# Performance work log

Hardware: AMD Instinct MI355X
Metric: run time of the kernel (lower is better)

## Reference

```python
import jax, jax.numpy as jnp
import numpy as np

B, S, H = 2, 256, 512
EPS = 1e-12  # TPLinker conditional LayerNorm default epsilon
NEG = -1e30  # finite stand-in for -inf in running max


def _cond_layer_norm(x, cond, Wg, Wb, gamma, beta):
    # TPLinker conditional LayerNorm: gamma/beta are modulated by a linear map of cond.
    g = gamma + cond @ Wg          # (..., H)
    b = beta + cond @ Wb           # (..., H)
    xc = x - jnp.mean(x, axis=-1, keepdims=True)
    inv = jax.lax.rsqrt(jnp.mean(xc * xc, axis=-1, keepdims=True) + EPS)
    return xc * inv * g + b


def setup_inputs() -> dict:
    key = jax.random.key(0)
    ks = jax.random.split(key, 6)
    return {
        "seq_hiddens": jax.random.normal(ks[0], (B, S, H), jnp.float32),
        "mask": jnp.ones((B, S), jnp.float32),
        "lamtha": jax.random.uniform(ks[1], (H,), jnp.float32),
        "Wg1": jax.random.normal(ks[2], (H, H), jnp.float32) * 0.02,
        "Wb1": jax.random.normal(ks[3], (H, H), jnp.float32) * 0.02,
        "g1": jnp.ones((H,), jnp.float32),
        "b1": jnp.zeros((H,), jnp.float32),
        "Wg2": jax.random.normal(ks[4], (H, H), jnp.float32) * 0.02,
        "Wb2": jax.random.normal(ks[5], (H, H), jnp.float32) * 0.02,
        "g2": jnp.ones((H,), jnp.float32),
        "b2": jnp.zeros((H,), jnp.float32),
    }


def reference(seq_hiddens, mask, lamtha, Wg1, Wb1, g1, b1, Wg2, Wb2, g2, b2):
    # mask additive penalty, broadcast over hidden (matches (1-mask)*-1000 expand)
    seq = seq_hiddens + ((1.0 - mask) * -1000.0)[:, :, None]  # (B,S,H)

    ii, jj = jnp.triu_indices(S)  # row-major pairs (i, j>=i), same order as the torch loop

    # window means over seq[i..j] via cumulative sums (replaces O(S^3) recomputation)
    csum = jnp.cumsum(seq, axis=1)                              # (B,S,H)
    lens = (jj - ii + 1).astype(seq.dtype)[None, :, None]
    mean_pairs = (csum[:, jj] - csum[:, ii] + seq[:, ii]) / lens  # (B,P,H)

    # window maxes over seq[i..j]: scan over j keeping running max per start i
    idx = jnp.arange(S)

    def step(state, j):
        sj = jnp.take(seq, j, axis=1)  # (B,H)
        new = jnp.where((idx <= j)[None, :, None],
                        jnp.maximum(state, sj[:, None, :]),
                        jnp.asarray(NEG, seq.dtype))
        return new, new

    _, Mall = jax.lax.scan(step, jnp.full((B, S, H), NEG, seq.dtype), idx)  # (S_j,B,S_i,H)
    max_pairs = Mall[jj, :, ii].transpose(1, 0, 2)  # (B,P,H)

    # mix pooling
    inner = lamtha * mean_pairs + (1.0 - lamtha) * max_pairs  # (B,P,H)

    visible = seq[:, jj]  # (B,P,H) token j
    repeat = seq[:, ii]   # (B,P,H) token i

    shaking = _cond_layer_norm(visible, repeat, Wg1, Wb1, g1, b1)
    return _cond_layer_norm(shaking, inner, Wg2, Wb2, g2, b2)
```

## Files before the change

kernel.cpp:

```cpp
#include <hip/hip_runtime.h>
#include <hip/hip_bf16.h>

typedef __hip_bfloat16 bf16;
typedef short short8 __attribute__((ext_vector_type(8)));
typedef float floatx4 __attribute__((ext_vector_type(4)));

#define S 256
#define H 512
#define P 32896
#define NROWS 65792
#define NEGF -1e30f
#define EPSF 1e-12f

#define OFF_SEQ    0u
#define OFF_LN1    2129920u
#define OFF_G1     3178496u
#define OFF_B1     4227072u
#define OFF_WCAT   5275648u
#define OFF_II     6324224u
#define OFF_JJ     6390016u
#define OFF_MU2    6455808u
#define OFF_INV2   6718976u
#define OFF_INNER  6982144u

__device__ __forceinline__ void gld_lds16(const void* g, void* l) {
    __builtin_amdgcn_global_load_lds(
        (const __attribute__((address_space(1))) void*)g,
        (__attribute__((address_space(3))) void*)l, 16, 0, 0);
}

__global__ __launch_bounds__(512) void fusedA_kernel(
    const float* __restrict__ x, const float* __restrict__ mask,
    float* __restrict__ seq, float* __restrict__ ln1,
    const float* __restrict__ Wg2, const float* __restrict__ Wb2,
    bf16* __restrict__ wcatT,
    unsigned short* __restrict__ ii, unsigned short* __restrict__ jj) {
    __shared__ float part[8][8][2];
    __shared__ float rstat[8][2];
    if (blockIdx.x < 64) {
        int b = blockIdx.x >> 5, sc = blockIdx.x & 31, h = threadIdx.x;
        int wave = h >> 6, lane = h & 63;
        int s0 = sc * 8;
        float v[8];
#pragma unroll
        for (int t = 0; t < 8; ++t) {
            int s = s0 + t;
            v[t] = x[(size_t)(b * S + s) * H + h] + (1.0f - mask[b * S + s]) * (-1000.0f);
            seq[(size_t)(b * S + s) * H + h] = v[t];
        }
#pragma unroll
        for (int t = 0; t < 8; ++t) {
            float s = v[t], q = v[t] * v[t];
            for (int o = 1; o < 64; o <<= 1) { s += __shfl_xor(s, o); q += __shfl_xor(q, o); }
            if (lane == 0) { part[wave][t][0] = s; part[wave][t][1] = q; }
        }
        __syncthreads();
        if (h < 16) {
            int row = h >> 1, st = h & 1;
            float a = 0.0f;
#pragma unroll
            for (int w = 0; w < 8; ++w) a += part[w][row][st];
            rstat[row][st] = a;
        }
        __syncthreads();
#pragma unroll
        for (int t = 0; t < 8; ++t) {
            float m = rstat[t][0] * (1.0f / 512.0f);
            float var = rstat[t][1] * (1.0f / 512.0f) - m * m;
            var = var < 0.0f ? 0.0f : var;
            float inv = rsqrtf(var + EPSF);
            ln1[(size_t)(b * S + s0 + t) * H + h] = (v[t] - m) * inv;
        }
    } else {
        int n = blockIdx.x - 64;
        if (n < 1024) {
            int k = threadIdx.x;
            int tt = n >> 7, c = n & 127;
            int h = tt * 64 + (c & 63);
            float v = (c < 64) ? Wg2[(size_t)k * H + h] : Wb2[(size_t)k * H + h];
            wcatT[(size_t)n * H + k] = __float2bfloat16(v);
        } else {
            int p = (n - 1024) * 512 + threadIdx.x;
            if (p >= P) return;
            float disc = 513.0f * 513.0f - 8.0f * (float)p;
            int i = (int)((513.0f - sqrtf(disc)) * 0.5f);
            i = i < 0 ? 0 : (i > S - 1 ? S - 1 : i);
            while (i > 0 && (i * S - i * (i - 1) / 2) > p) --i;
            while (i < S - 1 && ((i + 1) * S - (i + 1) * i / 2) <= p) ++i;
            int off = i * S - i * (i - 1) / 2;
            ii[p] = (unsigned short)i;
            jj[p] = (unsigned short)(i + (p - off));
        }
    }
}

__global__ __launch_bounds__(256) void g1b1_kernel(
    const float* __restrict__ seq, const float* __restrict__ Wg1, const float* __restrict__ Wb1,
    const float* __restrict__ g1, const float* __restrict__ b1,
    float* __restrict__ G1, float* __restrict__ B1) {
    __shared__ float rowbuf[4][H];
    int grp = blockIdx.x;
    int mat = blockIdx.y;
    int tid = threadIdx.x;
    int h0 = tid, h1 = tid + 256;
    int r0 = grp * 4;
#pragma unroll
    for (int r = 0; r < 4; ++r) {
        rowbuf[r][h0] = seq[(size_t)(r0 + r) * H + h0];
        rowbuf[r][h1] = seq[(size_t)(r0 + r) * H + h1];
    }
    __syncthreads();
    const float* W = mat ? Wb1 : Wg1;
    float acc[4][2] = {{0, 0}, {0, 0}, {0, 0}, {0, 0}};
#pragma unroll 2
    for (int k4 = 0; k4 < 128; ++k4) {
        float4 a0 = ((const float4*)rowbuf[0])[k4];
        float4 a1 = ((const float4*)rowbuf[1])[k4];
        float4 a2 = ((const float4*)rowbuf[2])[k4];
        float4 a3 = ((const float4*)rowbuf[3])[k4];
        float w00 = W[(size_t)(k4 * 4 + 0) * H + h0], w01 = W[(size_t)(k4 * 4 + 0) * H + h1];
        float w10 = W[(size_t)(k4 * 4 + 1) * H + h0], w11 = W[(size_t)(k4 * 4 + 1) * H + h1];
        float w20 = W[(size_t)(k4 * 4 + 2) * H + h0], w21 = W[(size_t)(k4 * 4 + 2) * H + h1];
        float w30 = W[(size_t)(k4 * 4 + 3) * H + h0], w31 = W[(size_t)(k4 * 4 + 3) * H + h1];
        acc[0][0] += a0.x * w00 + a0.y * w10 + a0.z * w20 + a0.w * w30;
        acc[0][1] += a0.x * w01 + a0.y * w11 + a0.z * w21 + a0.w * w31;
        acc[1][0] += a1.x * w00 + a1.y * w10 + a1.z * w20 + a1.w * w30;
        acc[1][1] += a1.x * w01 + a1.y * w11 + a1.z * w21 + a1.w * w31;
        acc[2][0] += a2.x * w00 + a2.y * w10 + a2.z * w20 + a2.w * w30;
        acc[2][1] += a2.x * w01 + a2.y * w11 + a2.z * w21 + a2.w * w31;
        acc[3][0] += a3.x * w00 + a3.y * w10 + a3.z * w20 + a3.w * w30;
        acc[3][1] += a3.x * w01 + a3.y * w11 + a3.z * w21 + a3.w * w31;
    }
    float bias0 = (mat ? b1 : g1)[h0];
    float bias1 = (mat ? b1 : g1)[h1];
    float* dst = mat ? B1 : G1;
#pragma unroll
    for (int r = 0; r < 4; ++r) {
        dst[(size_t)(r0 + r) * H + h0] = acc[r][0] + bias0;
        dst[(size_t)(r0 + r) * H + h1] = acc[r][1] + bias1;
    }
}

__global__ __launch_bounds__(256) void inner_kernel(
    const float* __restrict__ seq, const float* __restrict__ lamtha,
    bf16* __restrict__ inner) {
    int id = blockIdx.x;
    int t = id & 255, b = id >> 8;
    int i = b ? (255 - t) : t;
    int h2 = threadIdx.x;
    float2 lam = ((const float2*)lamtha)[h2];
    float2 oml = {1.0f - lam.x, 1.0f - lam.y};
    const float2* seqb = (const float2*)(seq + (size_t)b * S * H);
    float2 mrun = {NEGF, NEGF};
    float2 srun = {0.0f, 0.0f};
    size_t base = (size_t)b * P + (size_t)(i * S - i * (i - 1) / 2);
    __hip_bfloat162* dst = (__hip_bfloat162*)inner;
    int j = i;
#define INNER_STEP(vv, jx)                                                 \
    {                                                                      \
        srun.x += vv.x;                                                    \
        srun.y += vv.y;                                                    \
        mrun.x = fmaxf(mrun.x, vv.x);                                      \
        mrun.y = fmaxf(mrun.y, vv.y);                                      \
        float rl = 1.0f / (float)((jx) - i + 1);                           \
        float mx = srun.x * rl;                                            \
        float my = srun.y * rl;                                            \
        __hip_bfloat162 o;                                                 \
        o.x = __float2bfloat16(lam.x * mx + oml.x * mrun.x);               \
        o.y = __float2bfloat16(lam.y * my + oml.y * mrun.y);               \
        dst[(base + (size_t)((jx) - i)) * 256 + h2] = o;                   \
    }
    for (; j + 4 <= S; j += 4) {
        float2 v0 = seqb[(j + 0) * 256 + h2];
        float2 v1 = seqb[(j + 1) * 256 + h2];
        float2 v2 = seqb[(j + 2) * 256 + h2];
        float2 v3 = seqb[(j + 3) * 256 + h2];
        INNER_STEP(v0, j + 0)
        INNER_STEP(v1, j + 1)
        INNER_STEP(v2, j + 2)
        INNER_STEP(v3, j + 3)
    }
    for (; j < S; ++j) {
        float2 v = seqb[j * 256 + h2];
        INNER_STEP(v, j)
    }
#undef INNER_STEP
}

__global__ void stats_kernel(const float* __restrict__ ln1, const float* __restrict__ G1,
                             const float* __restrict__ B1,
                             const unsigned short* __restrict__ ii,
                             const unsigned short* __restrict__ jj,
                             float* __restrict__ mu2, float* __restrict__ inv2) {
    int r = blockIdx.x * 4 + (threadIdx.x >> 6);
    int lane = threadIdx.x & 63;
    int b = (r >= P) ? 1 : 0;
    int p = r - b * P;
    int i = ii[p], j = jj[p];
    const float4* lp = (const float4*)(ln1 + (size_t)(b * S + j) * H);
    const float4* gp = (const float4*)(G1 + (size_t)(b * S + i) * H);
    const float4* bp = (const float4*)(B1 + (size_t)(b * S + i) * H);
    float sum = 0.0f, ss = 0.0f;
#pragma unroll
    for (int t = 0; t < 2; ++t) {
        int idx = t * 64 + lane;
        float4 a = lp[idx], g = gp[idx], bb = bp[idx];
        float v0 = a.x * g.x + bb.x, v1 = a.y * g.y + bb.y;
        float v2 = a.z * g.z + bb.z, v3 = a.w * g.w + bb.w;
        sum += (v0 + v1) + (v2 + v3);
        ss += (v0 * v0 + v1 * v1) + (v2 * v2 + v3 * v3);
    }
    for (int o = 1; o < 64; o <<= 1) { sum += __shfl_xor(sum, o); ss += __shfl_xor(ss, o); }
    if (lane == 0) {
        float m = sum * (1.0f / 512.0f);
        float var = ss * (1.0f / 512.0f) - m * m;
        var = var < 0.0f ? 0.0f : var;
        mu2[r] = m;
        inv2[r] = rsqrtf(var + EPSF);
    }
}

__global__ __launch_bounds__(256, 2) void gemm_kernel(
    const bf16* __restrict__ inner, const bf16* __restrict__ wcatT,
    const float* __restrict__ g2, const float* __restrict__ b2,
    const float* __restrict__ ln1, const float* __restrict__ G1, const float* __restrict__ B1,
    const unsigned short* __restrict__ ii, const unsigned short* __restrict__ jj,
    const float* __restrict__ mu2, const float* __restrict__ inv2,
    float* __restrict__ out) {
    extern __shared__ __align__(16) char smem[];

    const int tid = threadIdx.x;
    const int wave = tid >> 6, lane = tid & 63;
    const int q = lane >> 4, l15 = lane & 15;
    const int wm = wave & 1, wn = wave >> 1;

    const int id = blockIdx.x;
    int rb, t;
    if (id < 4096) { rb = (id >> 6) * 8 + (id & 7); t = (id >> 3) & 7; }
    else           { int w = id - 4096; rb = 512 + (w & 1); t = w >> 1; }
    const int R0 = rb * 128;

    const int srow = tid >> 3;
    const int sx8 = ((tid & 7) ^ (srow & 7)) * 8;
    const bf16* const Ag = inner + (size_t)(R0 + srow) * H + sx8;
    const bf16* const Bg = wcatT + (size_t)(t * 128 + srow) * H + sx8;

    char* const A0 = smem;
    char* const B0 = smem + 16384;
    char* const A1 = smem + 32768;
    char* const B1s = smem + 49152;

    floatx4 acc[4][4];
#pragma unroll
    for (int a = 0; a < 4; ++a)
#pragma unroll
        for (int c = 0; c < 4; ++c) acc[a][c] = (floatx4){0.f, 0.f, 0.f, 0.f};

    auto STAGE = [&](int kt, char* Ad, char* Bd) {
#pragma unroll
        for (int i2 = 0; i2 < 4; ++i2)
            gld_lds16(Ag + (size_t)i2 * 32 * H + kt * 64, Ad + i2 * 4096 + wave * 1024);
#pragma unroll
        for (int i2 = 0; i2 < 4; ++i2)
            gld_lds16(Bg + (size_t)i2 * 32 * H + kt * 64, Bd + i2 * 4096 + wave * 1024);
    };

    STAGE(0, A0, B0);
    STAGE(1, A1, B1s);
    asm volatile("s_waitcnt vmcnt(8)" ::: "memory");
    asm volatile("s_barrier" ::: "memory");

#pragma unroll
    for (int kt = 0; kt < 8; ++kt) {
        char* const As = (kt & 1) ? A1 : A0;
        char* const Bs = (kt & 1) ? B1s : B0;

        short8 bfr[4][2], af[4][2];
#pragma unroll
        for (int ks = 0; ks < 2; ++ks) {
#pragma unroll
            for (int fn = 0; fn < 4; ++fn) {
                int nr = (fn < 2 ? wn * 32 + fn * 16 : 64 + wn * 32 + (fn - 2) * 16) + l15;
                bfr[fn][ks] = *(const short8*)(Bs + nr * 128 + (((ks * 4 + q) ^ (l15 & 7)) << 4));
            }
#pragma unroll
            for (int fm = 0; fm < 4; ++fm) {
                int mr = wm * 64 + fm * 16 + l15;
                af[fm][ks] = *(const short8*)(As + mr * 128 + (((ks * 4 + q) ^ (l15 & 7)) << 4));
            }
        }

        __builtin_amdgcn_s_setprio(1);
#pragma unroll
        for (int fm = 0; fm < 4; ++fm)
#pragma unroll
            for (int fn = 0; fn < 4; ++fn)
                acc[fm][fn] = __builtin_amdgcn_mfma_f32_16x16x32_bf16(af[fm][0], bfr[fn][0], acc[fm][fn], 0, 0, 0);
        __builtin_amdgcn_s_setprio(0);

        if (kt < 6) {
            asm volatile("s_waitcnt lgkmcnt(0)" ::: "memory");
            asm volatile("s_barrier" ::: "memory");
            STAGE(kt + 2, As, Bs);
        }

        __builtin_amdgcn_s_setprio(1);
#pragma unroll
        for (int fm = 0; fm < 4; ++fm)
#pragma unroll
            for (int fn = 0; fn < 4; ++fn)
                acc[fm][fn] = __builtin_amdgcn_mfma_f32_16x16x32_bf16(af[fm][1], bfr[fn][1], acc[fm][fn], 0, 0, 0);
        __builtin_amdgcn_s_setprio(0);

        if (kt < 6) {
            asm volatile("s_waitcnt vmcnt(8)" ::: "memory");
            asm volatile("s_barrier" ::: "memory");
        } else if (kt == 6) {
            asm volatile("s_waitcnt vmcnt(0)" ::: "memory");
            asm volatile("s_barrier" ::: "memory");
        }
    }

    float g2v[2], b2v[2];
#pragma unroll
    for (int fg = 0; fg < 2; ++fg) {
        int h = t * 64 + wn * 32 + fg * 16 + l15;
        g2v[fg] = g2[h];
        b2v[fg] = b2[h];
    }
#pragma unroll
    for (int fm = 0; fm < 4; ++fm) {
#pragma unroll
        for (int r = 0; r < 4; ++r) {
            int m = wm * 64 + fm * 16 + q * 4 + r;
            int rg = R0 + m;
            int b = (rg >= P) ? 1 : 0;
            int p = rg - b * P;
            int i = ii[p], j = jj[p];
            float mu = mu2[rg], iv = inv2[rg];
            const float* lp = ln1 + (size_t)(b * S + j) * H + t * 64 + wn * 32;
            const float* gp = G1 + (size_t)(b * S + i) * H + t * 64 + wn * 32;
            const float* bp = B1 + (size_t)(b * S + i) * H + t * 64 + wn * 32;
            float* op = out + (size_t)rg * H + t * 64 + wn * 32;
#pragma unroll
            for (int fg = 0; fg < 2; ++fg) {
                int c = fg * 16 + l15;
                float s = (lp[c] * gp[c] + bp[c] - mu) * iv;
                float G2v = acc[fm][fg][r] + g2v[fg];
                float B2v = acc[fm][fg + 2][r] + b2v[fg];
                op[c] = s * G2v + B2v;
            }
        }
    }
}

extern "C" void kernel_launch(void* const* d_in, const int* in_sizes, int n_in,
                              void* d_out, int out_size, void* d_ws, size_t ws_size,
                              hipStream_t stream) {
    const float* x = (const float*)d_in[0];
    const float* mask = (const float*)d_in[1];
    const float* lamtha = (const float*)d_in[2];
    const float* Wg1 = (const float*)d_in[3];
    const float* Wb1 = (const float*)d_in[4];
    const float* g1 = (const float*)d_in[5];
    const float* b1 = (const float*)d_in[6];
    const float* Wg2 = (const float*)d_in[7];
    const float* Wb2 = (const float*)d_in[8];
    const float* g2 = (const float*)d_in[9];
    const float* b2 = (const float*)d_in[10];
    float* out = (float*)d_out;

    char* ws = (char*)d_ws;
    float* seq = (float*)(ws + OFF_SEQ);
    float* ln1 = (float*)(ws + OFF_LN1);
    float* G1 = (float*)(ws + OFF_G1);
    float* B1 = (float*)(ws + OFF_B1);
    bf16* wcatT = (bf16*)(ws + OFF_WCAT);
    unsigned short* iiA = (unsigned short*)(ws + OFF_II);
    unsigned short* jjA = (unsigned short*)(ws + OFF_JJ);
    float* mu2 = (float*)(ws + OFF_MU2);
    float* inv2 = (float*)(ws + OFF_INV2);
    bf16* inner = (bf16*)(ws + OFF_INNER);

    static bool attr_set = false;
    if (!attr_set) {
        hipFuncSetAttribute((const void*)gemm_kernel,
                            hipFuncAttributeMaxDynamicSharedMemorySize, 65536);
        attr_set = true;
    }

    hipLaunchKernelGGL(fusedA_kernel, dim3(1153), dim3(512), 0, stream,
                       x, mask, seq, ln1, Wg2, Wb2, wcatT, iiA, jjA);
    hipLaunchKernelGGL(g1b1_kernel, dim3(128, 2), dim3(256), 0, stream,
                       seq, Wg1, Wb1, g1, b1, G1, B1);
    hipLaunchKernelGGL(inner_kernel, dim3(512), dim3(256), 0, stream,
                       seq, lamtha, inner);
    hipLaunchKernelGGL(stats_kernel, dim3(16448), dim3(256), 0, stream,
                       ln1, G1, B1, iiA, jjA, mu2, inv2);
    hipLaunchKernelGGL(gemm_kernel, dim3(4112), dim3(256), 65536, stream,
                       inner, wcatT, g2, b2, ln1, G1, B1, iiA, jjA, mu2, inv2, out);
}
```

Before: 301.8 us.

## Drop seq buffer, recompute mask add inline, fuse inner and stats kernels

```diff
diff --git a/kernel.cpp b/kernel.cpp
--- a/kernel.cpp
+++ b/kernel.cpp
@@ -12,7 +12,6 @@
 #define NEGF -1e30f
 #define EPSF 1e-12f
 
-#define OFF_SEQ    0u
 #define OFF_LN1    2129920u
 #define OFF_G1     3178496u
 #define OFF_B1     4227072u
@@ -31,7 +30,7 @@
 
 __global__ __launch_bounds__(512) void fusedA_kernel(
     const float* __restrict__ x, const float* __restrict__ mask,
-    float* __restrict__ seq, float* __restrict__ ln1,
+    float* __restrict__ ln1,
     const float* __restrict__ Wg2, const float* __restrict__ Wb2,
     bf16* __restrict__ wcatT,
     unsigned short* __restrict__ ii, unsigned short* __restrict__ jj) {
@@ -46,7 +45,6 @@
         for (int t = 0; t < 8; ++t) {
             int s = s0 + t;
             v[t] = x[(size_t)(b * S + s) * H + h] + (1.0f - mask[b * S + s]) * (-1000.0f);
-            seq[(size_t)(b * S + s) * H + h] = v[t];
         }
 #pragma unroll
         for (int t = 0; t < 8; ++t) {
@@ -95,7 +93,8 @@
 }
 
 __global__ __launch_bounds__(256) void g1b1_kernel(
-    const float* __restrict__ seq, const float* __restrict__ Wg1, const float* __restrict__ Wb1,
+    const float* __restrict__ x, const float* __restrict__ mask,
+    const float* __restrict__ Wg1, const float* __restrict__ Wb1,
     const float* __restrict__ g1, const float* __restrict__ b1,
     float* __restrict__ G1, float* __restrict__ B1) {
     __shared__ float rowbuf[4][H];
@@ -106,8 +105,10 @@
     int r0 = grp * 4;
 #pragma unroll
     for (int r = 0; r < 4; ++r) {
-        rowbuf[r][h0] = seq[(size_t)(r0 + r) * H + h0];
-        rowbuf[r][h1] = seq[(size_t)(r0 + r) * H + h1];
+        int row = r0 + r;
+        float add = (1.0f - mask[row]) * (-1000.0f);
+        rowbuf[r][h0] = x[(size_t)row * H + h0] + add;
+        rowbuf[r][h1] = x[(size_t)row * H + h1] + add;
     }
     __syncthreads();
     const float* W = mat ? Wb1 : Wg1;
@@ -141,27 +142,40 @@
     }
 }
 
-__global__ __launch_bounds__(256) void inner_kernel(
-    const float* __restrict__ seq, const float* __restrict__ lamtha,
-    bf16* __restrict__ inner) {
+__global__ __launch_bounds__(256) void innerstats_kernel(
+    const float* __restrict__ x, const float* __restrict__ mask,
+    const float* __restrict__ lamtha,
+    const float* __restrict__ ln1, const float* __restrict__ G1,
+    const float* __restrict__ B1,
+    bf16* __restrict__ inner, float* __restrict__ mu2, float* __restrict__ inv2) {
+    __shared__ float maskadd[256];
     int id = blockIdx.x;
-    int t = id & 255, b = id >> 8;
+    int kind = id & 1, sub = id >> 1;
+    int t = sub & 255, b = sub >> 8;
     int i = b ? (255 - t) : t;
-    int h2 = threadIdx.x;
-    float2 lam = ((const float2*)lamtha)[h2];
-    float2 oml = {1.0f - lam.x, 1.0f - lam.y};
-    const float2* seqb = (const float2*)(seq + (size_t)b * S * H);
-    float2 mrun = {NEGF, NEGF};
-    float2 srun = {0.0f, 0.0f};
-    size_t base = (size_t)b * P + (size_t)(i * S - i * (i - 1) / 2);
-    __hip_bfloat162* dst = (__hip_bfloat162*)inner;
-    int j = i;
-#define INNER_STEP(vv, jx)                                                 \
+    int tid = threadIdx.x;
+    int off = i * S - i * (i - 1) / 2;
+
+    if (kind == 0) {
+        int h2 = tid;
+        maskadd[tid] = (1.0f - mask[b * S + tid]) * (-1000.0f);
+        __syncthreads();
+        float2 lam = ((const float2*)lamtha)[h2];
+        float2 oml = {1.0f - lam.x, 1.0f - lam.y};
+        const float2* xb = (const float2*)(x + (size_t)b * S * H);
+        float2 mrun = {NEGF, NEGF};
+        float2 srun = {0.0f, 0.0f};
+        size_t base = (size_t)b * P + (size_t)off;
+        __hip_bfloat162* dst = (__hip_bfloat162*)inner;
+        int j = i;
+#define INNER_STEP(xx, jx)                                                 \
     {                                                                      \
-        srun.x += vv.x;                                                    \
-        srun.y += vv.y;                                                    \
-        mrun.x = fmaxf(mrun.x, vv.x);                                      \
-        mrun.y = fmaxf(mrun.y, vv.y);                                      \
+        float ma = maskadd[jx];                                            \
+        float vx = xx.x + ma, vy = xx.y + ma;                              \
+        srun.x += vx;                                                      \
+        srun.y += vy;                                                      \
+        mrun.x = fmaxf(mrun.x, vx);                                        \
+        mrun.y = fmaxf(mrun.y, vy);                                        \
         float rl = 1.0f / (float)((jx) - i + 1);                           \
         float mx = srun.x * rl;                                            \
         float my = srun.y * rl;                                            \
@@ -170,53 +184,47 @@
         o.y = __float2bfloat16(lam.y * my + oml.y * mrun.y);               \
         dst[(base + (size_t)((jx) - i)) * 256 + h2] = o;                   \
     }
-    for (; j + 4 <= S; j += 4) {
-        float2 v0 = seqb[(j + 0) * 256 + h2];
-        float2 v1 = seqb[(j + 1) * 256 + h2];
-        float2 v2 = seqb[(j + 2) * 256 + h2];
-        float2 v3 = seqb[(j + 3) * 256 + h2];
-        INNER_STEP(v0, j + 0)
-        INNER_STEP(v1, j + 1)
-        INNER_STEP(v2, j + 2)
-        INNER_STEP(v3, j + 3)
-    }
-    for (; j < S; ++j) {
-        float2 v = seqb[j * 256 + h2];
-        INNER_STEP(v, j)
-    }
+        for (; j + 4 <= S; j += 4) {
+            float2 x0 = xb[(j + 0) * 256 + h2];
+            float2 x1 = xb[(j + 1) * 256 + h2];
+            float2 x2 = xb[(j + 2) * 256 + h2];
+            float2 x3 = xb[(j + 3) * 256 + h2];
+            INNER_STEP(x0, j + 0)
+            INNER_STEP(x1, j + 1)
+            INNER_STEP(x2, j + 2)
+            INNER_STEP(x3, j + 3)
+        }
+        for (; j < S; ++j) {
+            float2 xv = xb[j * 256 + h2];
+            INNER_STEP(xv, j)
+        }
 #undef INNER_STEP
-}
-
-__global__ void stats_kernel(const float* __restrict__ ln1, const float* __restrict__ G1,
-                             const float* __restrict__ B1,
-                             const unsigned short* __restrict__ ii,
-                             const unsigned short* __restrict__ jj,
-                             float* __restrict__ mu2, float* __restrict__ inv2) {
-    int r = blockIdx.x * 4 + (threadIdx.x >> 6);
-    int lane = threadIdx.x & 63;
-    int b = (r >= P) ? 1 : 0;
-    int p = r - b * P;
-    int i = ii[p], j = jj[p];
-    const float4* lp = (const float4*)(ln1 + (size_t)(b * S + j) * H);
-    const float4* gp = (const float4*)(G1 + (size_t)(b * S + i) * H);
-    const float4* bp = (const float4*)(B1 + (size_t)(b * S + i) * H);
-    float sum = 0.0f, ss = 0.0f;
-#pragma unroll
-    for (int t = 0; t < 2; ++t) {
-        int idx = t * 64 + lane;
-        float4 a = lp[idx], g = gp[idx], bb = bp[idx];
-        float v0 = a.x * g.x + bb.x, v1 = a.y * g.y + bb.y;
-        float v2 = a.z * g.z + bb.z, v3 = a.w * g.w + bb.w;
-        sum += (v0 + v1) + (v2 + v3);
-        ss += (v0 * v0 + v1 * v1) + (v2 * v2 + v3 * v3);
-    }
-    for (int o = 1; o < 64; o <<= 1) { sum += __shfl_xor(sum, o); ss += __shfl_xor(ss, o); }
-    if (lane == 0) {
-        float m = sum * (1.0f / 512.0f);
-        float var = ss * (1.0f / 512.0f) - m * m;
-        var = var < 0.0f ? 0.0f : var;
-        mu2[r] = m;
-        inv2[r] = rsqrtf(var + EPSF);
+    } else {
+        int wave = tid >> 6, lane = tid & 63;
+        const float4* gp = (const float4*)(G1 + (size_t)(b * S + i) * H);
+        const float4* bp = (const float4*)(B1 + (size_t)(b * S + i) * H);
+        float4 ga = gp[lane * 2], gb = gp[lane * 2 + 1];
+        float4 ba = bp[lane * 2], bb = bp[lane * 2 + 1];
+        for (int j = i + wave; j < S; j += 4) {
+            const float4* lp = (const float4*)(ln1 + (size_t)(b * S + j) * H);
+            float4 a0 = lp[lane * 2], a1 = lp[lane * 2 + 1];
+            float v0 = a0.x * ga.x + ba.x, v1 = a0.y * ga.y + ba.y;
+            float v2 = a0.z * ga.z + ba.z, v3 = a0.w * ga.w + ba.w;
+            float v4 = a1.x * gb.x + bb.x, v5 = a1.y * gb.y + bb.y;
+            float v6 = a1.z * gb.z + bb.z, v7 = a1.w * gb.w + bb.w;
+            float sum = ((v0 + v1) + (v2 + v3)) + ((v4 + v5) + (v6 + v7));
+            float ss = ((v0 * v0 + v1 * v1) + (v2 * v2 + v3 * v3)) +
+                       ((v4 * v4 + v5 * v5) + (v6 * v6 + v7 * v7));
+            for (int o = 1; o < 64; o <<= 1) { sum += __shfl_xor(sum, o); ss += __shfl_xor(ss, o); }
+            if (lane == 0) {
+                int r = b * P + off + (j - i);
+                float m = sum * (1.0f / 512.0f);
+                float var = ss * (1.0f / 512.0f) - m * m;
+                var = var < 0.0f ? 0.0f : var;
+                mu2[r] = m;
+                inv2[r] = rsqrtf(var + EPSF);
+            }
+        }
     }
 }
 
@@ -371,7 +379,6 @@
     float* out = (float*)d_out;
 
     char* ws = (char*)d_ws;
-    float* seq = (float*)(ws + OFF_SEQ);
     float* ln1 = (float*)(ws + OFF_LN1);
     float* G1 = (float*)(ws + OFF_G1);
     float* B1 = (float*)(ws + OFF_B1);
@@ -390,13 +397,11 @@
     }
 
     hipLaunchKernelGGL(fusedA_kernel, dim3(1153), dim3(512), 0, stream,
-                       x, mask, seq, ln1, Wg2, Wb2, wcatT, iiA, jjA);
+                       x, mask, ln1, Wg2, Wb2, wcatT, iiA, jjA);
     hipLaunchKernelGGL(g1b1_kernel, dim3(128, 2), dim3(256), 0, stream,
-                       seq, Wg1, Wb1, g1, b1, G1, B1);
-    hipLaunchKernelGGL(inner_kernel, dim3(512), dim3(256), 0, stream,
-                       seq, lamtha, inner);
-    hipLaunchKernelGGL(stats_kernel, dim3(16448), dim3(256), 0, stream,
-                       ln1, G1, B1, iiA, jjA, mu2, inv2);
+                       x, mask, Wg1, Wb1, g1, b1, G1, B1);
+    hipLaunchKernelGGL(innerstats_kernel, dim3(1024), dim3(256), 0, stream,
+                       x, mask, lamtha, ln1, G1, B1, inner, mu2, inv2);
     hipLaunchKernelGGL(gemm_kernel, dim3(4112), dim3(256), 65536, stream,
                        inner, wcatT, g2, b2, ln1, G1, B1, iiA, jjA, mu2, inv2, out);
 }
```

Result: no change. 301.5 us (-0.1%).
